# Kernel tuning notes

Measured on AMD Instinct MI355X. Metric: run time of the kernel, lower is better.

## Reference

```python
import jax, jax.numpy as jnp
import numpy as np

B, P, D = 256, 128, 768        # batch, property slots per sample, encoder hidden dim
E = 64                          # num_properties (number of adapter heads)
H = 256                         # adapter_hidden_dim
H2 = H // 2
O = 2                           # output_dim
LN_EPS = 1e-5
RES_W_ADPT, RES_W_BASE = 0.7, 0.3


def setup_inputs() -> dict:
    key = jax.random.key(0)
    ks = jax.random.split(key, 12)
    hidden_states = jax.random.normal(ks[0], (B, P, D), dtype=jnp.float32)
    base_output = jax.random.normal(ks[1], (B, P, O), dtype=jnp.float32)
    properties = jax.random.randint(ks[2], (B, P), 0, E, dtype=jnp.int64)
    mask = (jax.random.uniform(ks[3], (B, P)) > 0.1).astype(jnp.float32)
    # Stacked per-head adapter parameters (LayerNorm + 3 Linears per head)
    ln_g = jnp.ones((E, D), dtype=jnp.float32)
    ln_b = jnp.zeros((E, D), dtype=jnp.float32)
    W1 = jax.random.normal(ks[4], (E, D, H), dtype=jnp.float32) * (1.0 / np.sqrt(D))
    b1 = jnp.zeros((E, H), dtype=jnp.float32)
    W2 = jax.random.normal(ks[5], (E, H, H2), dtype=jnp.float32) * (1.0 / np.sqrt(H))
    b2 = jnp.zeros((E, H2), dtype=jnp.float32)
    W3 = jax.random.normal(ks[6], (E, H2, O), dtype=jnp.float32) * 0.01  # init std=0.01 per source
    b3 = jnp.zeros((E, O), dtype=jnp.float32)
    return {
        "hidden_states": hidden_states, "base_output": base_output,
        "properties": properties, "mask": mask,
        "ln_g": ln_g, "ln_b": ln_b, "W1": W1, "b1": b1,
        "W2": W2, "b2": b2, "W3": W3, "b3": b3,
    }


def reference(hidden_states, base_output, properties, mask,
              ln_g, ln_b, W1, b1, W2, b2, W3, b3):
    b, p, d = hidden_states.shape
    o = W3.shape[-1]
    x = hidden_states.reshape(-1, d)                        # [N, D]
    # LayerNorm statistics are head-independent; only gamma/beta differ per head
    mu = jnp.mean(x, axis=-1, keepdims=True)
    var = jnp.mean((x - mu) ** 2, axis=-1, keepdims=True)
    xhat = (x - mu) * jax.lax.rsqrt(var + LN_EPS)           # [N, D]
    flat_p = properties.reshape(-1)                         # [N]
    flat_m = mask.reshape(-1)                               # [N]

    def body(acc, inp):
        idx, g, bt, w1, bb1, w2, bb2, w3, bb3 = inp
        h = jax.nn.relu((xhat * g + bt) @ w1 + bb1)         # [N, H]  (dropout = identity in eval)
        h = jax.nn.relu(h @ w2 + bb2)                       # [N, H2]
        out = h @ w3 + bb3                                  # [N, O]
        sel = (flat_p == idx) & (flat_m > 0)
        return jnp.where(sel[:, None], out, acc), None

    e = W1.shape[0]
    acc0 = jnp.zeros((b * p, o), dtype=x.dtype)
    acc, _ = jax.lax.scan(
        body, acc0,
        (jnp.arange(e), ln_g, ln_b, W1, b1, W2, b2, W3, b3))
    out = acc.reshape(b, p, o)
    out = RES_W_ADPT * out + RES_W_BASE * base_output       # use_residual=True
    return out * mask[..., None]
```

## Files before the change

kernel.cpp:

```cpp
#include <hip/hip_runtime.h>
#include <stdint.h>

typedef unsigned short u16;
typedef unsigned int   u32;

#define NTOK   32768
#define GD     768
#define GH     256
#define GH2    128
#define GE     64

typedef __bf16 bf16x8 __attribute__((ext_vector_type(8)));
typedef float  f32x4  __attribute__((ext_vector_type(4)));
union Frag { uint4 u; bf16x8 b; };

__device__ __forceinline__ float bf2f(u16 h) {
  union { u32 u; float f; } v; v.u = ((u32)h) << 16; return v.f;
}
__device__ __forceinline__ u16 f2bf(float f) {
  union { float f; u32 u; } v; v.f = f;
  u32 r = (v.u + 0x7fffu + ((v.u >> 16) & 1u)) >> 16;
  return (u16)r;
}

__device__ __forceinline__ void async16(void* lds, const void* g) {
  __builtin_amdgcn_global_load_lds(
      (const __attribute__((address_space(1))) void*)g,
      (__attribute__((address_space(3))) void*)lds, 16, 0, 0);
}

__device__ __forceinline__ int getProp(const int* p32, int t, int is64) {
  return is64 ? p32[2 * t] : p32[t];
}

static const size_t OFF_Y    = 0;
static const size_t OFF_W1T  = 50331648;
static const size_t OFF_W2T  = 75497472;
static const size_t OFF_TOK  = 79691776;
static const size_t OFF_META = 79822848;

__global__ void prep_kernel(u32* __restrict__ outz, int* __restrict__ meta) {
  int t = blockIdx.x * 256 + threadIdx.x;
  outz[t] = 0u;
  if (t < 4096) meta[t] = 0;
}

__global__ void prop_probe(const int* __restrict__ p32, int* __restrict__ flag) {
  const int ln = threadIdx.x;
  int v = 0;
#pragma unroll
  for (int j = 0; j < 8; ++j) v |= p32[2 * (ln * 8 + j) + 1];
#pragma unroll
  for (int d = 1; d < 64; d <<= 1) v |= __shfl_xor(v, d);
  if (ln == 0) *flag = (v == 0) ? 1 : 0;
}

__global__ void hist_kernel(const int* __restrict__ prop, const float* __restrict__ mask,
                            int* __restrict__ counts_p, const int* __restrict__ flag) {
  __shared__ int h[GE];
  const int tid = threadIdx.x;
  const int t = blockIdx.x * 256 + tid;
  if (tid < GE) h[tid] = 0;
  __syncthreads();
  if (mask[t] > 0.f) atomicAdd(&h[getProp(prop, t, *flag)], 1);
  __syncthreads();
  if (tid < GE && h[tid] > 0) atomicAdd(&counts_p[tid * 16], h[tid]);
}

__global__ void transpose_w1(const float* __restrict__ in, u16* __restrict__ out) {
  __shared__ u16 tl[64][260];
  const int bid = blockIdx.x;
  const int e  = bid / 12, r = bid % 12;
  const int d0 = (r / 4) * 256, h0 = (r % 4) * 64;
  const int tid = threadIdx.x;
  const size_t inMat = (size_t)e * GD * GH;
  const size_t outMat = (size_t)e * GH * GD;
  const int h_l = (tid & 15) * 4, d_l = tid >> 4;
#pragma unroll
  for (int dd = 0; dd < 16; ++dd) {
    const int d = d_l + dd * 16;
    float4 v = *(const float4*)(in + inMat + (size_t)(d0 + d) * GH + h0 + h_l);
    tl[h_l + 0][d] = f2bf(v.x);
    tl[h_l + 1][d] = f2bf(v.y);
    tl[h_l + 2][d] = f2bf(v.z);
    tl[h_l + 3][d] = f2bf(v.w);
  }
  __syncthreads();
  const int wv = tid >> 6, ln = tid & 63;
#pragma unroll
  for (int hh = 0; hh < 16; ++hh) {
    const int h = wv * 16 + hh;
    *(uint2*)(out + outMat + (size_t)(h0 + h) * GD + d0 + ln * 4) =
        *(const uint2*)&tl[h][ln * 4];
  }
}

__global__ void transpose_kernel(const float* __restrict__ in, u16* __restrict__ out,
                                 int R, int C, int tilesC) {
  __shared__ u16 tile[32][33];
  const int tilesPerMat = (R >> 5) * tilesC;
  const int e  = blockIdx.x / tilesPerMat;
  const int t  = blockIdx.x % tilesPerMat;
  const int tr = t / tilesC, tc = t % tilesC;
  const size_t mat = (size_t)e * R * C;
  const int tx = threadIdx.x & 31, ty = threadIdx.x >> 5;
  const int r0 = tr * 32, c0 = tc * 32;
#pragma unroll
  for (int i = 0; i < 32; i += 8)
    tile[ty + i][tx] = f2bf(in[mat + (size_t)(r0 + ty + i) * C + c0 + tx]);
  __syncthreads();
#pragma unroll
  for (int i = 0; i < 32; i += 8)
    out[mat + (size_t)(c0 + ty + i) * R + r0 + tx] = tile[tx][ty + i];
}

__global__ void ln_kernel(const float* __restrict__ hs, const float* __restrict__ g,
                          const float* __restrict__ bta, const int* __restrict__ prop,
                          u16* __restrict__ y, const int* __restrict__ flag) {
  const int wv = threadIdx.x >> 6, ln = threadIdx.x & 63;
  const int t = blockIdx.x * 4 + wv;
  const float* x = hs + (size_t)t * GD;
  float v[12];
  float s = 0.f, sq = 0.f;
#pragma unroll
  for (int c = 0; c < 3; ++c) {
    float4 u = *(const float4*)(x + c * 256 + ln * 4);
    v[c*4+0] = u.x; v[c*4+1] = u.y; v[c*4+2] = u.z; v[c*4+3] = u.w;
    s  += u.x + u.y + u.z + u.w;
    sq += u.x*u.x + u.y*u.y + u.z*u.z + u.w*u.w;
  }
#pragma unroll
  for (int d = 1; d < 64; d <<= 1) { s += __shfl_xor(s, d); sq += __shfl_xor(sq, d); }
  const float mu = s * (1.f / 768.f);
  const float rstd = rsqrtf(sq * (1.f / 768.f) - mu * mu + 1e-5f);
  const int p = getProp(prop, t, *flag);
  const float* gp = g + (size_t)p * GD;
  const float* bp = bta + (size_t)p * GD;
  u16* yp = y + (size_t)t * GD;
#pragma unroll
  for (int c = 0; c < 3; ++c) {
    float4 ug = *(const float4*)(gp + c * 256 + ln * 4);
    float4 ub = *(const float4*)(bp + c * 256 + ln * 4);
    float y0 = (v[c*4+0] - mu) * rstd * ug.x + ub.x;
    float y1 = (v[c*4+1] - mu) * rstd * ug.y + ub.y;
    float y2 = (v[c*4+2] - mu) * rstd * ug.z + ub.z;
    float y3 = (v[c*4+3] - mu) * rstd * ug.w + ub.w;
    uint2 o;
    o.x = (u32)f2bf(y0) | ((u32)f2bf(y1) << 16);
    o.y = (u32)f2bf(y2) | ((u32)f2bf(y3) << 16);
    *(uint2*)(yp + c * 256 + ln * 4) = o;
  }
}

__global__ void scan_kernel(const int* __restrict__ counts_p, int* __restrict__ offsets,
                            int* __restrict__ tileHead, int* __restrict__ tileRow,
                            int* __restrict__ nTilesPtr) {
  const int e = threadIdx.x;
  int c = counts_p[e * 16];
  int inc = c;
#pragma unroll
  for (int d = 1; d < 64; d <<= 1) { int n = __shfl_up(inc, d); if (e >= d) inc += n; }
  const int off = inc - c;
  offsets[e] = off;
  if (e == 63) offsets[64] = inc;
  int ntile = (c + 127) >> 7;
  int inct = ntile;
#pragma unroll
  for (int d = 1; d < 64; d <<= 1) { int n = __shfl_up(inct, d); if (e >= d) inct += n; }
  const int tb = inct - ntile;
  for (int j = 0; j < ntile; ++j) { tileHead[tb + j] = e; tileRow[tb + j] = off + j * 128; }
  if (e == 63) *nTilesPtr = inct;
}

__global__ void scatter_kernel(const int* __restrict__ prop, const float* __restrict__ mask,
                               const int* __restrict__ offsets, int* __restrict__ cursors_p,
                               int* __restrict__ tokenIds, const int* __restrict__ flag) {
  __shared__ int h[GE];
  __shared__ int basebin[GE];
  const int tid = threadIdx.x;
  const int t = blockIdx.x * 256 + tid;
  if (tid < GE) h[tid] = 0;
  __syncthreads();
  int p = -1, rank = 0;
  if (mask[t] > 0.f) {
    p = getProp(prop, t, *flag);
    rank = atomicAdd(&h[p], 1);
  }
  __syncthreads();
  if (tid < GE && h[tid] > 0) basebin[tid] = atomicAdd(&cursors_p[tid * 16], h[tid]);
  __syncthreads();
  if (p >= 0) tokenIds[offsets[p] + basebin[p] + rank] = t;
}

__global__ __launch_bounds__(256, 1) void adapter_gemm(
    const u16* __restrict__ y, const u16* __restrict__ w1t, const u16* __restrict__ w2t,
    const float* __restrict__ b1, const float* __restrict__ b2,
    const float* __restrict__ w3, const float* __restrict__ b3,
    const float* __restrict__ base, const float* __restrict__ mask,
    const int* __restrict__ tokenIds, const int* __restrict__ offsets,
    const int* __restrict__ tileHead, const int* __restrict__ tileRow,
    const int* __restrict__ nTilesPtr, float* __restrict__ outp) {
  __shared__ u16 sA[128 * 32];
  __shared__ u16 sH[128 * 136];
  __shared__ u16 sB[128 * 32];
  __shared__ float sBias1[256];
  __shared__ float sBias2[128];
  __shared__ float sW3[2][128];
  __shared__ float sB3[2];
  __shared__ int   sTok[128];

  const int tid  = threadIdx.x;
  const int wv   = tid >> 6;
  const int l15  = tid & 15;
  const int quad = (tid & 63) >> 4;
  const int arow = tid >> 2;
  const int koff = (tid & 3) * 8;
  const f32x4 vzero = {0.f, 0.f, 0.f, 0.f};
  const int nt = *nTilesPtr;

  for (int tile = blockIdx.x; tile < nt; tile += gridDim.x) {
    __syncthreads();
    const int e  = tileHead[tile];
    const int rs = tileRow[tile];
    const int nRows = min(128, offsets[e + 1] - rs);

    if (tid < 128) sTok[tid] = tokenIds[rs + min(tid, nRows - 1)];
    sBias1[tid] = b1[e * GH + tid];
    if (tid < 128) sBias2[tid] = b2[e * GH2 + tid];
    { const int k = tid >> 1, o = tid & 1; sW3[o][k] = w3[e * GH2 * 2 + k * 2 + o]; }
    if (tid < 2) sB3[tid] = b3[e * 2 + tid];
    __syncthreads();

    const u16* yrow0 = y + (size_t)sTok[arow] * GD;
    const u16* yrow1 = y + (size_t)sTok[64 + arow] * GD;
    const u16* w1e = w1t + (size_t)e * GH * GD;
    const u16* w2e = w2t + (size_t)e * GH2 * GH;

    f32x4 acc2[8][2];
#pragma unroll
    for (int f = 0; f < 8; ++f)
#pragma unroll
      for (int g = 0; g < 2; ++g) acc2[f][g] = vzero;

    for (int c = 0; c < 2; ++c) {
      f32x4 acc1[8][2];
#pragma unroll
      for (int f = 0; f < 8; ++f)
#pragma unroll
        for (int g = 0; g < 2; ++g) acc1[f][g] = vzero;

      for (int kt = 0; kt < 24; ++kt) {
        const int k0 = kt * 32;
        async16(sA + wv * 512,        yrow0 + k0 + koff);
        async16(sA + 2048 + wv * 512, yrow1 + k0 + koff);
#pragma unroll
        for (int j = 0; j < 2; ++j)
          async16(sB + j * 2048 + wv * 512,
                  w1e + (size_t)(c * 128 + j * 64 + arow) * GD + k0 + koff);
        __syncthreads();

        Frag fa[8], fb[2];
#pragma unroll
        for (int f = 0; f < 8; ++f)
          fa[f].u = *(const uint4*)&sA[(f * 16 + l15) * 32 + quad * 8];
#pragma unroll
        for (int g = 0; g < 2; ++g)
          fb[g].u = *(const uint4*)&sB[(wv * 32 + g * 16 + l15) * 32 + quad * 8];
#pragma unroll
        for (int f = 0; f < 8; ++f)
#pragma unroll
          for (int g = 0; g < 2; ++g)
            acc1[f][g] = __builtin_amdgcn_mfma_f32_16x16x32_bf16(fa[f].b, fb[g].b, acc1[f][g], 0, 0, 0);
        __syncthreads();
      }

#pragma unroll
      for (int f = 0; f < 8; ++f)
#pragma unroll
        for (int g = 0; g < 2; ++g) {
          const int col = wv * 32 + g * 16 + l15;
          const float bias = sBias1[c * 128 + col];
#pragma unroll
          for (int r = 0; r < 4; ++r) {
            const int row = f * 16 + quad * 4 + r;
            sH[row * 136 + col] = f2bf(fmaxf(acc1[f][g][r] + bias, 0.f));
          }
        }
      __syncthreads();

      for (int kt = 0; kt < 4; ++kt) {
        const int k0 = kt * 32;
#pragma unroll
        for (int j = 0; j < 2; ++j)
          async16(sB + j * 2048 + wv * 512,
                  w2e + (size_t)(j * 64 + arow) * GH + c * 128 + k0 + koff);
        __syncthreads();

        Frag fa2[8], fb2[2];
#pragma unroll
        for (int f = 0; f < 8; ++f)
          fa2[f].u = *(const uint4*)&sH[(f * 16 + l15) * 136 + k0 + quad * 8];
#pragma unroll
        for (int g = 0; g < 2; ++g)
          fb2[g].u = *(const uint4*)&sB[(wv * 32 + g * 16 + l15) * 32 + quad * 8];
#pragma unroll
        for (int f = 0; f < 8; ++f)
#pragma unroll
          for (int g = 0; g < 2; ++g)
            acc2[f][g] = __builtin_amdgcn_mfma_f32_16x16x32_bf16(fa2[f].b, fb2[g].b, acc2[f][g], 0, 0, 0);
        __syncthreads();
      }
    }

#pragma unroll
    for (int f = 0; f < 8; ++f)
#pragma unroll
      for (int g = 0; g < 2; ++g) {
        const int col = wv * 32 + g * 16 + l15;
        const float bias = sBias2[col];
#pragma unroll
        for (int r = 0; r < 4; ++r) {
          const int row = f * 16 + quad * 4 + r;
          sH[row * 136 + col] = f2bf(fmaxf(acc2[f][g][r] + bias, 0.f));
        }
      }
    __syncthreads();

    const int m = tid >> 1, o = tid & 1;
    if (m < nRows) {
      float a = sB3[o];
      const u16* h2row = &sH[m * 136];
#pragma unroll 16
      for (int k = 0; k < 128; ++k) a += bf2f(h2row[k]) * sW3[o][k];
      const int t = sTok[m];
      const float mk = mask[t];
      const float bs = base[t * 2 + o];
      outp[t * 2 + o] = (0.7f * a + 0.3f * bs) * mk;
    }
  }
}

extern "C" void kernel_launch(void* const* d_in, const int* in_sizes, int n_in,
                              void* d_out, int out_size, void* d_ws, size_t ws_size,
                              hipStream_t stream) {
  const float* hs   = (const float*)d_in[0];
  const float* base = (const float*)d_in[1];
  const int*   prop = (const int*)d_in[2];
  const float* mask = (const float*)d_in[3];
  const float* lng  = (const float*)d_in[4];
  const float* lnb  = (const float*)d_in[5];
  const float* W1   = (const float*)d_in[6];
  const float* b1   = (const float*)d_in[7];
  const float* W2   = (const float*)d_in[8];
  const float* b2   = (const float*)d_in[9];
  const float* W3   = (const float*)d_in[10];
  const float* b3   = (const float*)d_in[11];

  char* ws = (char*)d_ws;
  u16* y    = (u16*)(ws + OFF_Y);
  u16* w1t  = (u16*)(ws + OFF_W1T);
  u16* w2t  = (u16*)(ws + OFF_W2T);
  int* tok  = (int*)(ws + OFF_TOK);
  int* meta = (int*)(ws + OFF_META);
  int* counts_p  = meta;
  int* cursors_p = meta + 1024;
  int* offsets   = meta + 2048;
  int* tileHead  = meta + 2176;
  int* tileRow   = meta + 2688;
  int* nTiles    = meta + 3200;
  int* propFlag  = meta + 3201;

  prep_kernel<<<256, 256, 0, stream>>>((u32*)d_out, meta);
  prop_probe<<<1, 64, 0, stream>>>(prop, propFlag);
  hist_kernel<<<NTOK / 256, 256, 0, stream>>>(prop, mask, counts_p, propFlag);
  transpose_w1<<<768, 256, 0, stream>>>(W1, w1t);
  transpose_kernel<<<64 * 8 * 4, 256, 0, stream>>>(W2, w2t, GH, GH2, 4);
  ln_kernel<<<NTOK / 4, 256, 0, stream>>>(hs, lng, lnb, prop, y, propFlag);
  scan_kernel<<<1, 64, 0, stream>>>(counts_p, offsets, tileHead, tileRow, nTiles);
  scatter_kernel<<<NTOK / 256, 256, 0, stream>>>(prop, mask, offsets, cursors_p, tok, propFlag);
  adapter_gemm<<<256, 256, 0, stream>>>(y, w1t, w2t, b1, b2, W3, b3, base, mask,
                                        tok, offsets, tileHead, tileRow, nTiles,
                                        (float*)d_out);
}
```

Before: 287.9 us.

## Double-buffer GEMM LDS tiles, run two blocks per CU, merge setup kernels

The adapter GEMM now double-buffers its A/B tiles and W2 tiles in LDS. Each next K-slice is issued asynchronously before the current slice's MFMAs, which drops one barrier per iteration. LDS use is kept low by placing the layer-1 staging buffers and the hidden activation buffer in a union, so launch bounds can allow two blocks per CU and the grid doubles to 512. The prep, probe and histogram kernels are merged into one setup kernel that writes per-block counts without global atomics, and the scan sums those counts. In exchange, register pressure rises under the two-block bound and the scan kernel does more serial work.

Result: no change. 284.8 us (-1.1%).

```diff
diff --git a/kernel.cpp b/kernel.cpp
--- a/kernel.cpp
+++ b/kernel.cpp
@@ -39,32 +39,28 @@
 static const size_t OFF_TOK  = 79691776;
 static const size_t OFF_META = 79822848;
 
-__global__ void prep_kernel(u32* __restrict__ outz, int* __restrict__ meta) {
-  int t = blockIdx.x * 256 + threadIdx.x;
-  outz[t] = 0u;
-  if (t < 4096) meta[t] = 0;
-}
-
-__global__ void prop_probe(const int* __restrict__ p32, int* __restrict__ flag) {
-  const int ln = threadIdx.x;
-  int v = 0;
-#pragma unroll
-  for (int j = 0; j < 8; ++j) v |= p32[2 * (ln * 8 + j) + 1];
-#pragma unroll
-  for (int d = 1; d < 64; d <<= 1) v |= __shfl_xor(v, d);
-  if (ln == 0) *flag = (v == 0) ? 1 : 0;
-}
-
-__global__ void hist_kernel(const int* __restrict__ prop, const float* __restrict__ mask,
-                            int* __restrict__ counts_p, const int* __restrict__ flag) {
+__global__ void setup_kernel(const int* __restrict__ prop, const float* __restrict__ mask,
+                             u32* __restrict__ outz, int* __restrict__ counts2d,
+                             int* __restrict__ cursors_p, int* __restrict__ flagp) {
   __shared__ int h[GE];
+  __shared__ int vOr;
+  const int b = blockIdx.x;
   const int tid = threadIdx.x;
-  const int t = blockIdx.x * 256 + tid;
+  outz[b * 512 + tid] = 0u;
+  outz[b * 512 + 256 + tid] = 0u;
+  if (b < 4) cursors_p[b * 256 + tid] = 0;
   if (tid < GE) h[tid] = 0;
-  __syncthreads();
-  if (mask[t] > 0.f) atomicAdd(&h[getProp(prop, t, *flag)], 1);
-  __syncthreads();
-  if (tid < GE && h[tid] > 0) atomicAdd(&counts_p[tid * 16], h[tid]);
+  if (tid == 0) vOr = 0;
+  __syncthreads();
+  int v = prop[2 * tid + 1] | prop[2 * (tid + 256) + 1];
+  if (v) atomicOr(&vOr, 1);
+  __syncthreads();
+  const int is64 = (vOr == 0) ? 1 : 0;
+  if (b == 0 && tid == 0) *flagp = is64;
+  const int t = b * 256 + tid;
+  if (mask[t] > 0.f) atomicAdd(&h[getProp(prop, t, is64)], 1);
+  __syncthreads();
+  if (tid < GE) counts2d[b * GE + tid] = h[tid];
 }
 
 __global__ void transpose_w1(const float* __restrict__ in, u16* __restrict__ out) {
@@ -152,11 +148,12 @@
   }
 }
 
-__global__ void scan_kernel(const int* __restrict__ counts_p, int* __restrict__ offsets,
+__global__ void scan_kernel(const int* __restrict__ counts2d, int* __restrict__ offsets,
                             int* __restrict__ tileHead, int* __restrict__ tileRow,
                             int* __restrict__ nTilesPtr) {
   const int e = threadIdx.x;
-  int c = counts_p[e * 16];
+  int c = 0;
+  for (int b = 0; b < 128; ++b) c += counts2d[b * GE + e];
   int inc = c;
 #pragma unroll
   for (int d = 1; d < 64; d <<= 1) { int n = __shfl_up(inc, d); if (e >= d) inc += n; }
@@ -192,7 +189,7 @@
   if (p >= 0) tokenIds[offsets[p] + basebin[p] + rank] = t;
 }
 
-__global__ __launch_bounds__(256, 1) void adapter_gemm(
+__global__ __launch_bounds__(256, 2) void adapter_gemm(
     const u16* __restrict__ y, const u16* __restrict__ w1t, const u16* __restrict__ w2t,
     const float* __restrict__ b1, const float* __restrict__ b2,
     const float* __restrict__ w3, const float* __restrict__ b3,
@@ -200,9 +197,11 @@
     const int* __restrict__ tokenIds, const int* __restrict__ offsets,
     const int* __restrict__ tileHead, const int* __restrict__ tileRow,
     const int* __restrict__ nTilesPtr, float* __restrict__ outp) {
-  __shared__ u16 sA[128 * 32];
-  __shared__ u16 sH[128 * 136];
-  __shared__ u16 sB[128 * 32];
+  __shared__ union LU {
+    u16 g1[4][4096];
+    u16 h[17408];
+  } uni;
+  __shared__ u16 sB2[2][4096];
   __shared__ float sBias1[256];
   __shared__ float sBias2[128];
   __shared__ float sW3[2][128];
@@ -249,30 +248,50 @@
 #pragma unroll
         for (int g = 0; g < 2; ++g) acc1[f][g] = vzero;
 
+      {
+        u16* a = uni.g1[0]; u16* bb = uni.g1[2];
+        async16(a + wv * 512,        yrow0 + koff);
+        async16(a + 2048 + wv * 512, yrow1 + koff);
+#pragma unroll
+        for (int j = 0; j < 2; ++j)
+          async16(bb + j * 2048 + wv * 512,
+                  w1e + (size_t)(c * 128 + j * 64 + arow) * GD + koff);
+      }
+
       for (int kt = 0; kt < 24; ++kt) {
-        const int k0 = kt * 32;
-        async16(sA + wv * 512,        yrow0 + k0 + koff);
-        async16(sA + 2048 + wv * 512, yrow1 + k0 + koff);
-#pragma unroll
-        for (int j = 0; j < 2; ++j)
-          async16(sB + j * 2048 + wv * 512,
-                  w1e + (size_t)(c * 128 + j * 64 + arow) * GD + k0 + koff);
         __syncthreads();
-
+        if (kt + 1 < 24) {
+          const int k0 = (kt + 1) * 32;
+          const int par = (kt + 1) & 1;
+          u16* a = uni.g1[par]; u16* bb = uni.g1[2 + par];
+          async16(a + wv * 512,        yrow0 + k0 + koff);
+          async16(a + 2048 + wv * 512, yrow1 + k0 + koff);
+#pragma unroll
+          for (int j = 0; j < 2; ++j)
+            async16(bb + j * 2048 + wv * 512,
+                    w1e + (size_t)(c * 128 + j * 64 + arow) * GD + k0 + koff);
+        }
+        const int par = kt & 1;
+        const u16* a = uni.g1[par]; const u16* bb = uni.g1[2 + par];
         Frag fa[8], fb[2];
 #pragma unroll
         for (int f = 0; f < 8; ++f)
-          fa[f].u = *(const uint4*)&sA[(f * 16 + l15) * 32 + quad * 8];
+          fa[f].u = *(const uint4*)&a[(f * 16 + l15) * 32 + quad * 8];
 #pragma unroll
         for (int g = 0; g < 2; ++g)
-          fb[g].u = *(const uint4*)&sB[(wv * 32 + g * 16 + l15) * 32 + quad * 8];
+          fb[g].u = *(const uint4*)&bb[(wv * 32 + g * 16 + l15) * 32 + quad * 8];
 #pragma unroll
         for (int f = 0; f < 8; ++f)
 #pragma unroll
           for (int g = 0; g < 2; ++g)
             acc1[f][g] = __builtin_amdgcn_mfma_f32_16x16x32_bf16(fa[f].b, fb[g].b, acc1[f][g], 0, 0, 0);
-        __syncthreads();
       }
+      __syncthreads();
+
+#pragma unroll
+      for (int j = 0; j < 2; ++j)
+        async16(sB2[0] + j * 2048 + wv * 512,
+                w2e + (size_t)(j * 64 + arow) * GH + c * 128 + koff);
 
 #pragma unroll
       for (int f = 0; f < 8; ++f)
@@ -283,33 +302,35 @@
 #pragma unroll
           for (int r = 0; r < 4; ++r) {
             const int row = f * 16 + quad * 4 + r;
-            sH[row * 136 + col] = f2bf(fmaxf(acc1[f][g][r] + bias, 0.f));
+            uni.h[row * 136 + col] = f2bf(fmaxf(acc1[f][g][r] + bias, 0.f));
           }
         }
-      __syncthreads();
 
       for (int kt = 0; kt < 4; ++kt) {
-        const int k0 = kt * 32;
-#pragma unroll
-        for (int j = 0; j < 2; ++j)
-          async16(sB + j * 2048 + wv * 512,
-                  w2e + (size_t)(j * 64 + arow) * GH + c * 128 + k0 + koff);
         __syncthreads();
-
+        if (kt + 1 < 4) {
+          const int k0 = (kt + 1) * 32;
+          const int par = (kt + 1) & 1;
+#pragma unroll
+          for (int j = 0; j < 2; ++j)
+            async16(sB2[par] + j * 2048 + wv * 512,
+                    w2e + (size_t)(j * 64 + arow) * GH + c * 128 + k0 + koff);
+        }
+        const int par = kt & 1;
         Frag fa2[8], fb2[2];
 #pragma unroll
         for (int f = 0; f < 8; ++f)
-          fa2[f].u = *(const uint4*)&sH[(f * 16 + l15) * 136 + k0 + quad * 8];
+          fa2[f].u = *(const uint4*)&uni.h[(f * 16 + l15) * 136 + kt * 32 + quad * 8];
 #pragma unroll
         for (int g = 0; g < 2; ++g)
-          fb2[g].u = *(const uint4*)&sB[(wv * 32 + g * 16 + l15) * 32 + quad * 8];
+          fb2[g].u = *(const uint4*)&sB2[par][(wv * 32 + g * 16 + l15) * 32 + quad * 8];
 #pragma unroll
         for (int f = 0; f < 8; ++f)
 #pragma unroll
           for (int g = 0; g < 2; ++g)
             acc2[f][g] = __builtin_amdgcn_mfma_f32_16x16x32_bf16(fa2[f].b, fb2[g].b, acc2[f][g], 0, 0, 0);
-        __syncthreads();
       }
+      __syncthreads();
     }
 
 #pragma unroll
@@ -321,7 +342,7 @@
 #pragma unroll
         for (int r = 0; r < 4; ++r) {
           const int row = f * 16 + quad * 4 + r;
-          sH[row * 136 + col] = f2bf(fmaxf(acc2[f][g][r] + bias, 0.f));
+          uni.h[row * 136 + col] = f2bf(fmaxf(acc2[f][g][r] + bias, 0.f));
         }
       }
     __syncthreads();
@@ -329,7 +350,7 @@
     const int m = tid >> 1, o = tid & 1;
     if (m < nRows) {
       float a = sB3[o];
-      const u16* h2row = &sH[m * 136];
+      const u16* h2row = &uni.h[m * 136];
 #pragma unroll 16
       for (int k = 0; k < 128; ++k) a += bf2f(h2row[k]) * sW3[o][k];
       const int t = sTok[m];
@@ -362,23 +383,22 @@
   u16* w2t  = (u16*)(ws + OFF_W2T);
   int* tok  = (int*)(ws + OFF_TOK);
   int* meta = (int*)(ws + OFF_META);
-  int* counts_p  = meta;
-  int* cursors_p = meta + 1024;
-  int* offsets   = meta + 2048;
-  int* tileHead  = meta + 2176;
-  int* tileRow   = meta + 2688;
-  int* nTiles    = meta + 3200;
-  int* propFlag  = meta + 3201;
-
-  prep_kernel<<<256, 256, 0, stream>>>((u32*)d_out, meta);
-  prop_probe<<<1, 64, 0, stream>>>(prop, propFlag);
-  hist_kernel<<<NTOK / 256, 256, 0, stream>>>(prop, mask, counts_p, propFlag);
+  int* counts2d  = meta;
+  int* offsets   = meta + 8192;
+  int* tileHead  = meta + 8320;
+  int* tileRow   = meta + 8832;
+  int* nTiles    = meta + 9344;
+  int* propFlag  = meta + 9345;
+  int* cursors_p = meta + 10240;
+
+  setup_kernel<<<128, 256, 0, stream>>>(prop, mask, (u32*)d_out, counts2d,
+                                        cursors_p, propFlag);
   transpose_w1<<<768, 256, 0, stream>>>(W1, w1t);
   transpose_kernel<<<64 * 8 * 4, 256, 0, stream>>>(W2, w2t, GH, GH2, 4);
   ln_kernel<<<NTOK / 4, 256, 0, stream>>>(hs, lng, lnb, prop, y, propFlag);
-  scan_kernel<<<1, 64, 0, stream>>>(counts_p, offsets, tileHead, tileRow, nTiles);
+  scan_kernel<<<1, 64, 0, stream>>>(counts2d, offsets, tileHead, tileRow, nTiles);
   scatter_kernel<<<NTOK / 256, 256, 0, stream>>>(prop, mask, offsets, cursors_p, tok, propFlag);
-  adapter_gemm<<<256, 256, 0, stream>>>(y, w1t, w2t, b1, b2, W3, b3, base, mask,
+  adapter_gemm<<<512, 256, 0, stream>>>(y, w1t, w2t, b1, b2, W3, b3, base, mask,
                                         tok, offsets, tileHead, tileRow, nTiles,
                                         (float*)d_out);
 }
```
